# Optimization experiments

Measured on AMD Instinct MI355X. Metric: run time of the kernel, lower is better.

## Reference

```python
import jax, jax.numpy as jnp
import numpy as np

N = 10000        # num_nodes
F_IN = 256       # dataset_num_features
H = 128          # hidden_channels
C_OUT = 40       # dataset_num_classes
L = 3            # num_layers
HEADS = 8
DH = H // HEADS  # per-head dim
E = 160000       # num edges (before self loops)
SCALE = 1.0 / float(np.sqrt(DH))


def setup_inputs() -> dict:
    key = jax.random.key(0)
    ks = jax.random.split(key, 8)
    s = lambda k, *sh: (jax.random.normal(k, sh, dtype=jnp.float32) * 0.05)
    return dict(
        edge_index=jax.random.randint(ks[0], (2, E), 0, N, dtype=jnp.int32),
        x_param=s(ks[1], N, F_IN),
        lin1_w=s(ks[2], F_IN, H),
        lin1_b=jnp.zeros((H,), jnp.float32),
        wq=s(ks[3], L, H, H),
        wk=s(ks[4], L, H, H),
        wv=s(ks[5], L, H, H),
        bq=jnp.zeros((L, H), jnp.float32),
        bk=jnp.zeros((L, H), jnp.float32),
        bv=jnp.zeros((L, H), jnp.float32),
        lin2_w=s(ks[6], H, C_OUT),
        lin2_b=jnp.zeros((C_OUT,), jnp.float32),
    )


def _gcn_norm(edge_index):
    # PyG gcn_norm: add self loops (weight 1), symmetric D^-1/2 A D^-1/2
    loops = jnp.arange(N, dtype=edge_index.dtype)
    row = jnp.concatenate([edge_index[0], loops])  # source j
    col = jnp.concatenate([edge_index[1], loops])  # target i
    deg = jax.ops.segment_sum(jnp.ones(row.shape, jnp.float32), col, num_segments=N)
    dis = jnp.where(deg > 0, jax.lax.rsqrt(jnp.maximum(deg, 1e-12)), 0.0)
    return row, col, dis[row] * dis[col]


def _restricted_softmax(score):
    # softmax with an implicit extra logit at `margin=0`
    m = jnp.maximum(jnp.max(score, axis=-1, keepdims=True), 0.0)
    e = jnp.exp(score - m)
    return e / (jnp.sum(e, axis=-1, keepdims=True) + jnp.exp(-m))


def _forward(edge_index, x_param, lin1_w, lin1_b, wq, wk, wv, bq, bk, bv, lin2_w, lin2_b):
    row, col, norm = _gcn_norm(edge_index)
    # dropouts are eval-mode no-ops
    x = jax.nn.relu(x_param @ lin1_w + lin1_b)  # [N, H]
    x_all = x[:, None, :]                       # [N, 1, H]
    for l in range(L):
        t = x_all.shape[1]
        # project per-node first (linear commutes with per-edge gather)
        q = (x_all[:, -1] @ wq[l] + bq[l]).reshape(N, HEADS, DH)      # query from latest state
        k = (x_all @ wk[l] + bk[l]).reshape(N, t, HEADS, DH)          # keys over full history
        v = (x_all @ wv[l] + bv[l]).reshape(N, t, HEADS, DH)
        qe = q[col]   # [Etot, heads, dh]   (x_i)
        ke = k[row]   # [Etot, t, heads, dh] (x_j)
        ve = v[row]
        score = jnp.einsum('ehd,ethd->eht', qe, ke) * SCALE
        attn = _restricted_softmax(score)        # attention-dropout is a no-op in eval
        msg = jnp.einsum('eht,ethd->ehd', attn, ve).reshape(-1, H) * norm[:, None]
        out = jax.ops.segment_sum(msg, col, num_segments=N)  # aggr='add'
        x = jax.nn.relu(out)
        x_all = jnp.concatenate([x_all, x[:, None, :]], axis=1)
    logits = x_all[:, -1] @ lin2_w + lin2_b
    return jax.nn.log_softmax(logits, axis=1)


def reference(edge_index, x_param, lin1_w, lin1_b, wq, wk, wv, bq, bk, bv, lin2_w, lin2_b):
    return _forward(edge_index, x_param, lin1_w, lin1_b, wq, wk, wv, bq, bk, bv, lin2_w, lin2_b)
```

## Files before the change

kernel.cpp:

```cpp
#include <hip/hip_runtime.h>
#include <math.h>

#define N_NODES 10000
#define F_IN_D  256
#define H_DIM   128
#define C_OUTD  40
#define NHEADS  8
#define NEDGES  160000
#define ETOT    (NEDGES + N_NODES)
#define SCALE_F 0.25f
#define TILES_N 157
#define KVSZ    ((size_t)N_NODES * 3 * 256)

typedef __attribute__((ext_vector_type(8))) short bf16x8;
typedef __attribute__((ext_vector_type(4))) float f32x4;
typedef __attribute__((ext_vector_type(2))) float f32x2;

__device__ __forceinline__ unsigned short f2bf(float f) {
    unsigned int u = __float_as_uint(f);
    unsigned int r = (u + 0x7FFFu + ((u >> 16) & 1u)) >> 16;
    return (unsigned short)r;
}
__device__ __forceinline__ unsigned char f2fp8(float v) {
    int pk = __builtin_amdgcn_cvt_pk_fp8_f32(v, v, 0, false);
    return (unsigned char)(pk & 0xff);
}


__global__ void k_prep(const float* __restrict__ w1, const float* __restrict__ wq,
                       const float* __restrict__ wk, const float* __restrict__ wv,
                       const float* __restrict__ w2, const int* __restrict__ col,
                       unsigned short* __restrict__ W1T, unsigned short* __restrict__ WTq,
                       unsigned short* __restrict__ WTk, unsigned short* __restrict__ WTv,
                       unsigned short* __restrict__ W2T, int* __restrict__ degi) {
    int b = blockIdx.x;
    if (b < 728) {
        int e = b * 256 + threadIdx.x;
        if (e < 32768) {
            int n = e >> 8, k = e & 255;
            W1T[e] = f2bf(w1[k * H_DIM + n]);
        } else if (e < 180224) {
            int e2 = e - 32768;
            int mat = e2 >> 14;
            int r   = e2 & 16383;
            int n = r >> 7, k = r & 127;
            int l = mat / 3, ws = mat % 3;
            const float*    src = (ws == 0) ? wq  : (ws == 1) ? wk  : wv;
            unsigned short* dst = (ws == 0) ? WTq : (ws == 1) ? WTk : WTv;
            dst[l * 16384 + n * H_DIM + k] = f2bf(src[l * 16384 + k * H_DIM + n]);
        } else if (e < 186368) {
            int e3 = e - 180224;
            int c = e3 >> 7, k = e3 & 127;
            W2T[c * H_DIM + k] = (c < C_OUTD) ? f2bf(w2[k * C_OUTD + c]) : 0;
        }
    } else {
        int e = (b - 728) * 256 + threadIdx.x;
        if (e < NEDGES) atomicAdd(&degi[col[e]], 1);
    }
}


__device__ __forceinline__ void lin1_block(int bid, int ct0, const float* __restrict__ X,
                                           const unsigned short* __restrict__ W1T,
                                           const float* __restrict__ b1,
                                           unsigned short* __restrict__ X0, int nct) {
    int tid = threadIdx.x;
    int wid = tid >> 6, lane = tid & 63;
    int m = lane & 15, quad = lane >> 4;
    int rowA = bid * 64 + wid * 16 + m;
    int rowc = rowA < N_NODES ? rowA : N_NODES - 1;
    bf16x8 af[8];
    const float* ap = X + (size_t)rowc * F_IN_D + quad * 8;
    #pragma unroll
    for (int s = 0; s < 8; ++s) {
        float4 lo = *(const float4*)(ap + s * 32);
        float4 hi = *(const float4*)(ap + s * 32 + 4);
        union { unsigned short u[8]; bf16x8 v; } pk;
        pk.u[0] = f2bf(lo.x); pk.u[1] = f2bf(lo.y);
        pk.u[2] = f2bf(lo.z); pk.u[3] = f2bf(lo.w);
        pk.u[4] = f2bf(hi.x); pk.u[5] = f2bf(hi.y);
        pk.u[6] = f2bf(hi.z); pk.u[7] = f2bf(hi.w);
        af[s] = pk.v;
    }
    int row0 = bid * 64 + wid * 16 + quad * 4;
    for (int ct = ct0; ct < ct0 + nct; ++ct) {
        int col = ct * 16 + m;
        const unsigned short* bp = W1T + (size_t)col * F_IN_D + quad * 8;
        f32x4 acc = {0.f, 0.f, 0.f, 0.f};
        #pragma unroll
        for (int s = 0; s < 8; ++s) {
            bf16x8 bfr = __builtin_bit_cast(bf16x8, *(const uint4*)(bp + s * 32));
            acc = __builtin_amdgcn_mfma_f32_16x16x32_bf16(af[s], bfr, acc, 0, 0, 0);
        }
        float bb = b1[col];
        #pragma unroll
        for (int rg = 0; rg < 4; ++rg) {
            int r = row0 + rg;
            if (r < N_NODES)
                X0[(size_t)r * H_DIM + col] = f2bf(fmaxf(acc[rg] + bb, 0.f));
        }
    }
}

__device__ __forceinline__ void qkv_block(int mi, int rt,
                                          const unsigned short* __restrict__ XHb,
                                          const unsigned short* __restrict__ WTq_l,
                                          const unsigned short* __restrict__ WTk_l,
                                          const unsigned short* __restrict__ WTv_l,
                                          const float* __restrict__ bq_l,
                                          const float* __restrict__ bk_l,
                                          const float* __restrict__ bv_l,
                                          unsigned short* __restrict__ Qb,
                                          unsigned char* __restrict__ KVb,
                                          int hasQ, int qslice, int nK, int sbase, int nct) {
    int tid = threadIdx.x;
    int wid = tid >> 6, lane = tid & 63;
    int m = lane & 15, quad = lane >> 4;
    const unsigned short* WT; const float* bias; int slice, mode;
    if (hasQ && mi == 0) { WT = WTq_l; bias = bq_l; slice = qslice; mode = 0; }
    else {
        int j = mi - hasQ;
        if (j < nK) { WT = WTk_l; bias = bk_l; slice = sbase + j;      mode = 1; }
        else        { WT = WTv_l; bias = bv_l; slice = sbase + j - nK; mode = 2; }
    }
    const unsigned short* A = XHb + (size_t)slice * N_NODES * H_DIM;
    int rowA = rt * 64 + wid * 16 + m;
    bf16x8 af[4];
    const unsigned short* ap = A + (size_t)rowA * H_DIM + quad * 8;
    #pragma unroll
    for (int s = 0; s < 4; ++s)
        af[s] = __builtin_bit_cast(bf16x8, *(const uint4*)(ap + s * 32));
    int row0 = rt * 64 + wid * 16 + quad * 4;
    int vofs = (mode == 2) ? 8 : 0;
    for (int cp = 0; cp < nct; ++cp) {
        int colA = cp * 32 + m;
        int colB = colA + 16;
        const unsigned short* bpA = WT + (size_t)colA * H_DIM + quad * 8;
        const unsigned short* bpB = WT + (size_t)colB * H_DIM + quad * 8;
        bf16x8 bA[4], bB[4];
        #pragma unroll
        for (int s = 0; s < 4; ++s) {
            bA[s] = __builtin_bit_cast(bf16x8, *(const uint4*)(bpA + s * 32));
            bB[s] = __builtin_bit_cast(bf16x8, *(const uint4*)(bpB + s * 32));
        }
        f32x4 accA = {0.f, 0.f, 0.f, 0.f};
        f32x4 accB = {0.f, 0.f, 0.f, 0.f};
        #pragma unroll
        for (int s = 0; s < 4; ++s) {
            accA = __builtin_amdgcn_mfma_f32_16x16x32_bf16(af[s], bA[s], accA, 0, 0, 0);
            accB = __builtin_amdgcn_mfma_f32_16x16x32_bf16(af[s], bB[s], accB, 0, 0, 0);
        }
        float bbA = bias[colA], bbB = bias[colB];
        #pragma unroll
        for (int rg = 0; rg < 4; ++rg) {
            int r = row0 + rg;
            if (r < N_NODES) {
                float vA = accA[rg] + bbA;
                float vB = accB[rg] + bbB;
                if (mode == 0) {
                    Qb[(size_t)r * H_DIM + colA] = f2bf(vA * SCALE_F);
                    Qb[(size_t)r * H_DIM + colB] = f2bf(vB * SCALE_F);
                } else {
                    size_t nb = ((size_t)r * 3 + slice) * 256;
                    KVb[nb + (colA >> 3) * 16 + (colA & 7) + vofs] = f2fp8(vA);
                    KVb[nb + (colB >> 3) * 16 + (colB & 7) + vofs] = f2fp8(vB);
                }
            }
        }
    }
}


template <int T>
__device__ __forceinline__ void kv_load(const uint4* __restrict__ KV, int r, int ci,
                                        uint4 (&kv)[T]) {
    const uint4* p = KV + (size_t)r * 48 + ci;
    #pragma unroll
    for (int s = 0; s < T; ++s) kv[s] = p[s * 16];
}

template <int T>
__device__ __forceinline__ void edge_accum(const uint4 (&kv)[T], const float (&q)[8],
                                           float nrm, float (&a)[8]) {
    float den = 1.f;
    float mv[8];
    #pragma unroll
    for (int i = 0; i < 8; ++i) mv[i] = 0.f;
    #pragma unroll
    for (int s = 0; s < T; ++s) {
        f32x2 k0 = __builtin_amdgcn_cvt_pk_f32_fp8(kv[s].x, false);
        f32x2 k1 = __builtin_amdgcn_cvt_pk_f32_fp8(kv[s].x, true);
        f32x2 k2 = __builtin_amdgcn_cvt_pk_f32_fp8(kv[s].y, false);
        f32x2 k3 = __builtin_amdgcn_cvt_pk_f32_fp8(kv[s].y, true);
        float p = q[0] * k0[0] + q[1] * k0[1] + q[2] * k1[0] + q[3] * k1[1]
                + q[4] * k2[0] + q[5] * k2[1] + q[6] * k3[0] + q[7] * k3[1];
        p += __shfl_xor(p, 1, 2);
        float w = __expf(p);
        den += w;
        f32x2 v0 = __builtin_amdgcn_cvt_pk_f32_fp8(kv[s].z, false);
        f32x2 v1 = __builtin_amdgcn_cvt_pk_f32_fp8(kv[s].z, true);
        f32x2 v2 = __builtin_amdgcn_cvt_pk_f32_fp8(kv[s].w, false);
        f32x2 v3 = __builtin_amdgcn_cvt_pk_f32_fp8(kv[s].w, true);
        mv[0] += w * v0[0]; mv[1] += w * v0[1];
        mv[2] += w * v1[0]; mv[3] += w * v1[1];
        mv[4] += w * v2[0]; mv[5] += w * v2[1];
        mv[6] += w * v3[0]; mv[7] += w * v3[1];
    }
    float ws = __fdividef(nrm, den);
    #pragma unroll
    for (int i = 0; i < 8; ++i) a[i] += ws * mv[i];
}

template <int T>
__device__ __forceinline__ void attn_block(int bid, const unsigned short* __restrict__ Q,
                                           const uint4* __restrict__ KV,
                                           const int2* __restrict__ csr,
                                           const int* __restrict__ degi,
                                           unsigned int* __restrict__ Xout) {
    int tid = threadIdx.x;
    int wid = tid >> 6, lane = tid & 63;
    int quarter = lane >> 4, ci = lane & 15;
    int n = bid * 4 + wid;

    int cnt = degi[n] + 1;
    if (cnt > 64) cnt = 64;
    int li = lane < cnt ? lane : cnt - 1;
    int2 eAll = csr[(n << 6) + li];
    int   rAll = eAll.x;
    float nAll = (lane < cnt) ? __int_as_float(eAll.y) : 0.f;

    float q[8];
    {
        uint4 qp = *(const uint4*)&Q[(size_t)n * H_DIM + ci * 8];
        q[0] = __uint_as_float(qp.x << 16);
        q[1] = __uint_as_float(qp.x & 0xffff0000u);
        q[2] = __uint_as_float(qp.y << 16);
        q[3] = __uint_as_float(qp.y & 0xffff0000u);
        q[4] = __uint_as_float(qp.z << 16);
        q[5] = __uint_as_float(qp.z & 0xffff0000u);
        q[6] = __uint_as_float(qp.w << 16);
        q[7] = __uint_as_float(qp.w & 0xffff0000u);
    }
    int nq = (cnt + 3) >> 2;
    float a[8];
    #pragma unroll
    for (int i = 0; i < 8; ++i) a[i] = 0.f;

    auto rowN = [&](int j4) { return __shfl(rAll, j4 < 63 ? j4 : 63, 64); };
    auto nrmN = [&](int j4) { return __shfl(nAll, j4 < 63 ? j4 : 63, 64); };

    uint4 kv0[T], kv1[T], kv2[T];
    kv_load<T>(KV, rowN(quarter), ci, kv0);
    kv_load<T>(KV, rowN(4 + quarter), ci, kv1);
    kv_load<T>(KV, rowN(8 + quarter), ci, kv2);

    int j = 0;
    for (;;) {
        edge_accum<T>(kv0, q, nrmN(j * 4 + quarter), a);
        if (++j >= nq) break;
        kv_load<T>(KV, rowN((j + 2) * 4 + quarter), ci, kv0);
        edge_accum<T>(kv1, q, nrmN(j * 4 + quarter), a);
        if (++j >= nq) break;
        kv_load<T>(KV, rowN((j + 2) * 4 + quarter), ci, kv1);
        edge_accum<T>(kv2, q, nrmN(j * 4 + quarter), a);
        if (++j >= nq) break;
        kv_load<T>(KV, rowN((j + 2) * 4 + quarter), ci, kv2);
    }

    #pragma unroll
    for (int i = 0; i < 8; ++i) {
        a[i] += __shfl_xor(a[i], 16, 64);
        a[i] += __shfl_xor(a[i], 32, 64);
    }
    if (quarter == 0) {
        uint4 o;
        o.x = ((unsigned int)f2bf(fmaxf(a[1], 0.f)) << 16) | (unsigned int)f2bf(fmaxf(a[0], 0.f));
        o.y = ((unsigned int)f2bf(fmaxf(a[3], 0.f)) << 16) | (unsigned int)f2bf(fmaxf(a[2], 0.f));
        o.z = ((unsigned int)f2bf(fmaxf(a[5], 0.f)) << 16) | (unsigned int)f2bf(fmaxf(a[4], 0.f));
        o.w = ((unsigned int)f2bf(fmaxf(a[7], 0.f)) << 16) | (unsigned int)f2bf(fmaxf(a[6], 0.f));
        *(uint4*)&Xout[(size_t)n * 64 + ci * 4] = o;
    }
}


__global__ __launch_bounds__(256) void k_lin1_scatter(const float* __restrict__ X,
                                                      const unsigned short* __restrict__ W1T,
                                                      const float* __restrict__ b1,
                                                      unsigned short* __restrict__ X0,
                                                      const int* __restrict__ row,
                                                      const int* __restrict__ col,
                                                      const int* __restrict__ degi,
                                                      int* __restrict__ cursor,
                                                      int2* __restrict__ csr, int nct) {
    int b = blockIdx.x;
    if (b < 2 * TILES_N) {
        int rt = b % TILES_N, half = b / TILES_N;
        lin1_block(rt, half * 4, X, W1T, b1, X0, nct);
        return;
    }
    int e = (b - 2 * TILES_N) * 256 + threadIdx.x;
    if (e >= ETOT) return;
    int r, c;
    if (e < NEDGES) { r = row[e]; c = col[e]; }
    else            { r = c = e - NEDGES; }
    int slot = atomicAdd(&cursor[c], 1);
    if (slot > 63) slot = 63;
    float dr = rsqrtf((float)(degi[r] + 1));
    float dc = rsqrtf((float)(degi[c] + 1));
    int2 ent; ent.x = r; ent.y = __float_as_int(dr * dc);
    csr[(c << 6) + slot] = ent;
}

template <int T>
__global__ __launch_bounds__(256) void k_attn_qkvold(const unsigned short* __restrict__ Q,
                                                     const uint4* __restrict__ KV,
                                                     const int2* __restrict__ csr,
                                                     const int* __restrict__ degi,
                                                     unsigned int* __restrict__ Xout,
                                                     const unsigned short* __restrict__ XHb,
                                                     const unsigned short* __restrict__ WTk_l,
                                                     const unsigned short* __restrict__ WTv_l,
                                                     const float* __restrict__ bk_l,
                                                     const float* __restrict__ bv_l,
                                                     unsigned char* __restrict__ KVnext,
                                                     int nK, int nct) {
    if (blockIdx.x < 2500) {
        attn_block<T>(blockIdx.x, Q, KV, csr, degi, Xout);
        return;
    }
    int b = blockIdx.x - 2500;
    qkv_block(b / TILES_N, b % TILES_N, XHb, nullptr, WTk_l, WTv_l,
              nullptr, bk_l, bv_l, nullptr, KVnext, 0, 0, nK, 0, nct);
}

__global__ __launch_bounds__(256) void k_qkv(const unsigned short* __restrict__ XHb,
                                             const unsigned short* __restrict__ WTq_l,
                                             const unsigned short* __restrict__ WTk_l,
                                             const unsigned short* __restrict__ WTv_l,
                                             const float* __restrict__ bq_l,
                                             const float* __restrict__ bk_l,
                                             const float* __restrict__ bv_l,
                                             unsigned short* __restrict__ Qb,
                                             unsigned char* __restrict__ KVb,
                                             int qslice, int nct) {
    qkv_block(blockIdx.x / TILES_N, blockIdx.x % TILES_N, XHb, WTq_l, WTk_l, WTv_l,
              bq_l, bk_l, bv_l, Qb, KVb, 1, qslice, 1, qslice, nct);
}

template <int T>
__global__ __launch_bounds__(256) void k_attn_agg(const unsigned short* __restrict__ Q,
                                                  const uint4* __restrict__ KV,
                                                  const int2* __restrict__ csr,
                                                  const int* __restrict__ degi,
                                                  unsigned int* __restrict__ Xout) {
    attn_block<T>(blockIdx.x, Q, KV, csr, degi, Xout);
}


__global__ __launch_bounds__(128) void k_lin2_mfma(const unsigned short* __restrict__ X,
                                                   const unsigned short* __restrict__ W2T,
                                                   const float* __restrict__ b2,
                                                   float* __restrict__ out) {
    int tid = threadIdx.x;
    int wid = tid >> 6, lane = tid & 63;
    int m = lane & 15, quad = lane >> 4;
    int rowA = blockIdx.x * 32 + wid * 16 + m;
    bf16x8 af[4];
    const unsigned short* ap = X + (size_t)rowA * H_DIM + quad * 8;
    #pragma unroll
    for (int s = 0; s < 4; ++s)
        af[s] = __builtin_bit_cast(bf16x8, *(const uint4*)(ap + s * 32));

    f32x4 acc0 = {0.f, 0.f, 0.f, 0.f};
    f32x4 acc1 = {0.f, 0.f, 0.f, 0.f};
    f32x4 acc2 = {0.f, 0.f, 0.f, 0.f};
    const unsigned short* bp0 = W2T + (size_t)(m)      * H_DIM + quad * 8;
    const unsigned short* bp1 = W2T + (size_t)(16 + m) * H_DIM + quad * 8;
    const unsigned short* bp2 = W2T + (size_t)(32 + m) * H_DIM + quad * 8;
    #pragma unroll
    for (int s = 0; s < 4; ++s) {
        bf16x8 b0 = __builtin_bit_cast(bf16x8, *(const uint4*)(bp0 + s * 32));
        acc0 = __builtin_amdgcn_mfma_f32_16x16x32_bf16(af[s], b0, acc0, 0, 0, 0);
        bf16x8 b1 = __builtin_bit_cast(bf16x8, *(const uint4*)(bp1 + s * 32));
        acc1 = __builtin_amdgcn_mfma_f32_16x16x32_bf16(af[s], b1, acc1, 0, 0, 0);
        bf16x8 b2f = __builtin_bit_cast(bf16x8, *(const uint4*)(bp2 + s * 32));
        acc2 = __builtin_amdgcn_mfma_f32_16x16x32_bf16(af[s], b2f, acc2, 0, 0, 0);
    }

    float bb0 = b2[m], bb1 = b2[16 + m];
    float bb2 = (m < 8) ? b2[32 + m] : 0.f;
    int row0 = blockIdx.x * 32 + wid * 16 + quad * 4;
    #pragma unroll
    for (int rg = 0; rg < 4; ++rg) {
        int r = row0 + rg;
        float v0 = acc0[rg] + bb0;
        float v1 = acc1[rg] + bb1;
        float v2 = (m < 8) ? (acc2[rg] + bb2) : -INFINITY;
        float mx = fmaxf(fmaxf(v0, v1), v2);
        #pragma unroll
        for (int o = 8; o > 0; o >>= 1) mx = fmaxf(mx, __shfl_xor(mx, o, 16));
        float sm = __expf(v0 - mx) + __expf(v1 - mx) + ((m < 8) ? __expf(v2 - mx) : 0.f);
        #pragma unroll
        for (int o = 8; o > 0; o >>= 1) sm += __shfl_xor(sm, o, 16);
        float lse = mx + __logf(sm);
        if (r < N_NODES) {
            out[(size_t)r * C_OUTD + m]      = v0 - lse;
            out[(size_t)r * C_OUTD + 16 + m] = v1 - lse;
            if (m < 8) out[(size_t)r * C_OUTD + 32 + m] = v2 - lse;
        }
    }
}


extern "C" void kernel_launch(void* const* d_in, const int* in_sizes, int n_in,
                              void* d_out, int out_size, void* d_ws, size_t ws_size,
                              hipStream_t stream) {
    const int*   ei      = (const int*)d_in[0];
    const int*   row     = ei;
    const int*   col     = ei + NEDGES;
    const float* x_param = (const float*)d_in[1];
    const float* lin1_w  = (const float*)d_in[2];
    const float* lin1_b  = (const float*)d_in[3];
    const float* wq      = (const float*)d_in[4];
    const float* wk      = (const float*)d_in[5];
    const float* wv      = (const float*)d_in[6];
    const float* bq      = (const float*)d_in[7];
    const float* bk      = (const float*)d_in[8];
    const float* bv      = (const float*)d_in[9];
    const float* lin2_w  = (const float*)d_in[10];
    const float* lin2_b  = (const float*)d_in[11];
    float*       out     = (float*)d_out;

    char* wbase = (char*)d_ws;
    size_t off = 0;
    auto alloc = [&](size_t bytes) -> void* {
        off = (off + 255) & ~(size_t)255;
        void* p = wbase + off;
        off += bytes;
        return p;
    };
    int*            degi     = (int*)           alloc((size_t)N_NODES * 4);
    int*            cursor   = (int*)           alloc((size_t)N_NODES * 4);
    int2*           csr      = (int2*)          alloc((size_t)N_NODES * 64 * 8);
    unsigned short* W1T      = (unsigned short*)alloc((size_t)H_DIM * F_IN_D * 2);
    unsigned short* WTq      = (unsigned short*)alloc((size_t)3 * H_DIM * H_DIM * 2);
    unsigned short* WTk      = (unsigned short*)alloc((size_t)3 * H_DIM * H_DIM * 2);
    unsigned short* WTv      = (unsigned short*)alloc((size_t)3 * H_DIM * H_DIM * 2);
    unsigned short* W2T      = (unsigned short*)alloc((size_t)48 * H_DIM * 2);
    unsigned short* XHb      = (unsigned short*)alloc((size_t)4 * N_NODES * H_DIM * 2);
    unsigned short* Qb       = (unsigned short*)alloc((size_t)N_NODES * H_DIM * 2);
    unsigned char*  KVb      = (unsigned char*) alloc(2 * KVSZ);

    hipMemsetAsync(degi, 0,
                   (size_t)((char*)(cursor + N_NODES) - (char*)degi), stream);
    k_prep<<<1353, 256, 0, stream>>>(lin1_w, wq, wk, wv, lin2_w, col,
                                     W1T, WTq, WTk, WTv, W2T, degi);

    k_lin1_scatter<<<2 * TILES_N + 665, 256, 0, stream>>>(
        x_param, W1T, lin1_b, XHb, row, col, degi, cursor, csr, 4);

    k_qkv<<<3 * TILES_N, 256, 0, stream>>>(
        XHb, WTq, WTk, WTv, bq, bk, bv, Qb, KVb, 0, 4);

    unsigned int* X1 = (unsigned int*)(XHb + (size_t)1 * N_NODES * H_DIM);
    unsigned int* X2 = (unsigned int*)(XHb + (size_t)2 * N_NODES * H_DIM);
    unsigned int* X3 = (unsigned int*)(XHb + (size_t)3 * N_NODES * H_DIM);

    k_attn_qkvold<1><<<2500 + 2 * TILES_N, 256, 0, stream>>>(
        Qb, (const uint4*)KVb, csr, degi, X1,
        XHb, WTk + 16384, WTv + 16384, bk + H_DIM, bv + H_DIM,
        KVb + KVSZ, 1, 4);

    k_qkv<<<3 * TILES_N, 256, 0, stream>>>(
        XHb, WTq + 16384, WTk + 16384, WTv + 16384,
        bq + H_DIM, bk + H_DIM, bv + H_DIM, Qb, KVb + KVSZ, 1, 4);

    k_attn_qkvold<2><<<2500 + 4 * TILES_N, 256, 0, stream>>>(
        Qb, (const uint4*)(KVb + KVSZ), csr, degi, X2,
        XHb, WTk + 2 * 16384, WTv + 2 * 16384, bk + 2 * H_DIM, bv + 2 * H_DIM,
        KVb, 2, 4);

    k_qkv<<<3 * TILES_N, 256, 0, stream>>>(
        XHb, WTq + 2 * 16384, WTk + 2 * 16384, WTv + 2 * 16384,
        bq + 2 * H_DIM, bk + 2 * H_DIM, bv + 2 * H_DIM, Qb, KVb, 2, 4);

    k_attn_agg<3><<<2500, 256, 0, stream>>>(Qb, (const uint4*)KVb, csr, degi, X3);

    k_lin2_mfma<<<313, 128, 0, stream>>>(XHb + (size_t)3 * N_NODES * H_DIM,
                                         W2T, lin2_b, out);
}
```

Measured before the change: 228.0 us.

## Fuse all stages into one persistent cooperative kernel with grid syncs

Replaces the sequence of nine kernel launches plus a memset with a single cooperative persistent kernel that loops over work units per stage and separates stages with grid-wide barriers. This removes per-launch overhead and the idle gaps between dependent kernels. In exchange, every stage runs on an occupancy-limited grid with grid.sync costs, and the larger fused kernel may use more registers and run at lower occupancy. The old multi-kernel path is kept as a fallback if the cooperative launch fails, and lin2 now uses 256-thread blocks.

```diff
diff --git a/kernel.cpp b/kernel.cpp
--- a/kernel.cpp
+++ b/kernel.cpp
@@ -1,5 +1,8 @@
 #include <hip/hip_runtime.h>
+#include <hip/hip_cooperative_groups.h>
 #include <math.h>
+
+namespace cg = cooperative_groups;
 
 #define N_NODES 10000
 #define F_IN_D  256
@@ -27,38 +30,61 @@
 }
 
 
-__global__ void k_prep(const float* __restrict__ w1, const float* __restrict__ wq,
-                       const float* __restrict__ wk, const float* __restrict__ wv,
-                       const float* __restrict__ w2, const int* __restrict__ col,
-                       unsigned short* __restrict__ W1T, unsigned short* __restrict__ WTq,
-                       unsigned short* __restrict__ WTk, unsigned short* __restrict__ WTv,
-                       unsigned short* __restrict__ W2T, int* __restrict__ degi) {
-    int b = blockIdx.x;
+struct MegaArgs {
+    const int* row; const int* col;
+    const float* x_param;
+    const float* w1; const float* b1;
+    const float* wq; const float* wk; const float* wv;
+    const float* bq; const float* bk; const float* bv;
+    const float* w2; const float* b2;
+    float* out;
+    int* degi; int* cursor; int2* csr;
+    unsigned short* W1T; unsigned short* WTq; unsigned short* WTk;
+    unsigned short* WTv; unsigned short* W2T; unsigned short* XHb;
+    unsigned short* Qb; unsigned char* KVb;
+    int nct;
+};
+
+
+__device__ __forceinline__ void prep_unit(int b, const MegaArgs& A) {
     if (b < 728) {
         int e = b * 256 + threadIdx.x;
         if (e < 32768) {
             int n = e >> 8, k = e & 255;
-            W1T[e] = f2bf(w1[k * H_DIM + n]);
+            A.W1T[e] = f2bf(A.w1[k * H_DIM + n]);
         } else if (e < 180224) {
             int e2 = e - 32768;
             int mat = e2 >> 14;
             int r   = e2 & 16383;
             int n = r >> 7, k = r & 127;
             int l = mat / 3, ws = mat % 3;
-            const float*    src = (ws == 0) ? wq  : (ws == 1) ? wk  : wv;
-            unsigned short* dst = (ws == 0) ? WTq : (ws == 1) ? WTk : WTv;
+            const float*    src = (ws == 0) ? A.wq  : (ws == 1) ? A.wk  : A.wv;
+            unsigned short* dst = (ws == 0) ? A.WTq : (ws == 1) ? A.WTk : A.WTv;
             dst[l * 16384 + n * H_DIM + k] = f2bf(src[l * 16384 + k * H_DIM + n]);
         } else if (e < 186368) {
             int e3 = e - 180224;
             int c = e3 >> 7, k = e3 & 127;
-            W2T[c * H_DIM + k] = (c < C_OUTD) ? f2bf(w2[k * C_OUTD + c]) : 0;
+            A.W2T[c * H_DIM + k] = (c < C_OUTD) ? f2bf(A.w2[k * C_OUTD + c]) : 0;
         }
     } else {
         int e = (b - 728) * 256 + threadIdx.x;
-        if (e < NEDGES) atomicAdd(&degi[col[e]], 1);
-    }
-}
-
+        if (e < NEDGES) atomicAdd(&A.degi[A.col[e]], 1);
+    }
+}
+
+__device__ __forceinline__ void scatter_unit(int su, const MegaArgs& A) {
+    int e = su * 256 + threadIdx.x;
+    if (e >= ETOT) return;
+    int r, c;
+    if (e < NEDGES) { r = A.row[e]; c = A.col[e]; }
+    else            { r = c = e - NEDGES; }
+    int slot = atomicAdd(&A.cursor[c], 1);
+    if (slot > 63) slot = 63;
+    float dr = rsqrtf((float)(A.degi[r] + 1));
+    float dc = rsqrtf((float)(A.degi[c] + 1));
+    int2 ent; ent.x = r; ent.y = __float_as_int(dr * dc);
+    A.csr[(c << 6) + slot] = ent;
+}
 
 __device__ __forceinline__ void lin1_block(int bid, int ct0, const float* __restrict__ X,
                                            const unsigned short* __restrict__ W1T,
@@ -282,89 +308,14 @@
     }
 }
 
-
-__global__ __launch_bounds__(256) void k_lin1_scatter(const float* __restrict__ X,
-                                                      const unsigned short* __restrict__ W1T,
-                                                      const float* __restrict__ b1,
-                                                      unsigned short* __restrict__ X0,
-                                                      const int* __restrict__ row,
-                                                      const int* __restrict__ col,
-                                                      const int* __restrict__ degi,
-                                                      int* __restrict__ cursor,
-                                                      int2* __restrict__ csr, int nct) {
-    int b = blockIdx.x;
-    if (b < 2 * TILES_N) {
-        int rt = b % TILES_N, half = b / TILES_N;
-        lin1_block(rt, half * 4, X, W1T, b1, X0, nct);
-        return;
-    }
-    int e = (b - 2 * TILES_N) * 256 + threadIdx.x;
-    if (e >= ETOT) return;
-    int r, c;
-    if (e < NEDGES) { r = row[e]; c = col[e]; }
-    else            { r = c = e - NEDGES; }
-    int slot = atomicAdd(&cursor[c], 1);
-    if (slot > 63) slot = 63;
-    float dr = rsqrtf((float)(degi[r] + 1));
-    float dc = rsqrtf((float)(degi[c] + 1));
-    int2 ent; ent.x = r; ent.y = __float_as_int(dr * dc);
-    csr[(c << 6) + slot] = ent;
-}
-
-template <int T>
-__global__ __launch_bounds__(256) void k_attn_qkvold(const unsigned short* __restrict__ Q,
-                                                     const uint4* __restrict__ KV,
-                                                     const int2* __restrict__ csr,
-                                                     const int* __restrict__ degi,
-                                                     unsigned int* __restrict__ Xout,
-                                                     const unsigned short* __restrict__ XHb,
-                                                     const unsigned short* __restrict__ WTk_l,
-                                                     const unsigned short* __restrict__ WTv_l,
-                                                     const float* __restrict__ bk_l,
-                                                     const float* __restrict__ bv_l,
-                                                     unsigned char* __restrict__ KVnext,
-                                                     int nK, int nct) {
-    if (blockIdx.x < 2500) {
-        attn_block<T>(blockIdx.x, Q, KV, csr, degi, Xout);
-        return;
-    }
-    int b = blockIdx.x - 2500;
-    qkv_block(b / TILES_N, b % TILES_N, XHb, nullptr, WTk_l, WTv_l,
-              nullptr, bk_l, bv_l, nullptr, KVnext, 0, 0, nK, 0, nct);
-}
-
-__global__ __launch_bounds__(256) void k_qkv(const unsigned short* __restrict__ XHb,
-                                             const unsigned short* __restrict__ WTq_l,
-                                             const unsigned short* __restrict__ WTk_l,
-                                             const unsigned short* __restrict__ WTv_l,
-                                             const float* __restrict__ bq_l,
-                                             const float* __restrict__ bk_l,
-                                             const float* __restrict__ bv_l,
-                                             unsigned short* __restrict__ Qb,
-                                             unsigned char* __restrict__ KVb,
-                                             int qslice, int nct) {
-    qkv_block(blockIdx.x / TILES_N, blockIdx.x % TILES_N, XHb, WTq_l, WTk_l, WTv_l,
-              bq_l, bk_l, bv_l, Qb, KVb, 1, qslice, 1, qslice, nct);
-}
-
-template <int T>
-__global__ __launch_bounds__(256) void k_attn_agg(const unsigned short* __restrict__ Q,
-                                                  const uint4* __restrict__ KV,
-                                                  const int2* __restrict__ csr,
-                                                  const int* __restrict__ degi,
-                                                  unsigned int* __restrict__ Xout) {
-    attn_block<T>(blockIdx.x, Q, KV, csr, degi, Xout);
-}
-
-
-__global__ __launch_bounds__(128) void k_lin2_mfma(const unsigned short* __restrict__ X,
-                                                   const unsigned short* __restrict__ W2T,
-                                                   const float* __restrict__ b2,
-                                                   float* __restrict__ out) {
+__device__ __forceinline__ void lin2_block(int bid, const unsigned short* __restrict__ X,
+                                           const unsigned short* __restrict__ W2T,
+                                           const float* __restrict__ b2,
+                                           float* __restrict__ out) {
     int tid = threadIdx.x;
     int wid = tid >> 6, lane = tid & 63;
     int m = lane & 15, quad = lane >> 4;
-    int rowA = blockIdx.x * 32 + wid * 16 + m;
+    int rowA = bid * 64 + wid * 16 + m;
     bf16x8 af[4];
     const unsigned short* ap = X + (size_t)rowA * H_DIM + quad * 8;
     #pragma unroll
@@ -389,7 +340,7 @@
 
     float bb0 = b2[m], bb1 = b2[16 + m];
     float bb2 = (m < 8) ? b2[32 + m] : 0.f;
-    int row0 = blockIdx.x * 32 + wid * 16 + quad * 4;
+    int row0 = bid * 64 + wid * 16 + quad * 4;
     #pragma unroll
     for (int rg = 0; rg < 4; ++rg) {
         int r = row0 + rg;
@@ -412,25 +363,129 @@
 }
 
 
+__global__ __launch_bounds__(256) void k_mega(MegaArgs A) {
+    cg::grid_group grid = cg::this_grid();
+    const int nb  = gridDim.x;
+    const int gt  = blockIdx.x * 256 + threadIdx.x;
+    const int gsz = nb * 256;
+
+    unsigned int* X1 = (unsigned int*)(A.XHb + (size_t)1 * N_NODES * H_DIM);
+    unsigned int* X2 = (unsigned int*)(A.XHb + (size_t)2 * N_NODES * H_DIM);
+    unsigned int* X3 = (unsigned int*)(A.XHb + (size_t)3 * N_NODES * H_DIM);
+
+    for (int i = gt; i < N_NODES; i += gsz) { A.degi[i] = 0; A.cursor[i] = 0; }
+    grid.sync();
+
+    for (int u = blockIdx.x; u < 1353; u += nb) prep_unit(u, A);
+    grid.sync();
+
+    for (int u = blockIdx.x; u < 979; u += nb) {
+        if (u < 314) lin1_block(u % TILES_N, (u / TILES_N) * 4,
+                                A.x_param, A.W1T, A.b1, A.XHb, A.nct);
+        else scatter_unit(u - 314, A);
+    }
+    grid.sync();
+
+    for (int u = blockIdx.x; u < 471; u += nb)
+        qkv_block(u / TILES_N, u % TILES_N, A.XHb, A.WTq, A.WTk, A.WTv,
+                  A.bq, A.bk, A.bv, A.Qb, A.KVb, 1, 0, 1, 0, A.nct);
+    grid.sync();
+
+    for (int u = blockIdx.x; u < 2814; u += nb) {
+        if (u < 2500) attn_block<1>(u, A.Qb, (const uint4*)A.KVb, A.csr, A.degi, X1);
+        else {
+            int b = u - 2500;
+            qkv_block(b / TILES_N, b % TILES_N, A.XHb, nullptr,
+                      A.WTk + 16384, A.WTv + 16384, nullptr,
+                      A.bk + H_DIM, A.bv + H_DIM, nullptr,
+                      A.KVb + KVSZ, 0, 0, 1, 0, A.nct);
+        }
+    }
+    grid.sync();
+
+    for (int u = blockIdx.x; u < 471; u += nb)
+        qkv_block(u / TILES_N, u % TILES_N, A.XHb,
+                  A.WTq + 16384, A.WTk + 16384, A.WTv + 16384,
+                  A.bq + H_DIM, A.bk + H_DIM, A.bv + H_DIM,
+                  A.Qb, A.KVb + KVSZ, 1, 1, 1, 1, A.nct);
+    grid.sync();
+
+    for (int u = blockIdx.x; u < 3128; u += nb) {
+        if (u < 2500) attn_block<2>(u, A.Qb, (const uint4*)(A.KVb + KVSZ),
+                                    A.csr, A.degi, X2);
+        else {
+            int b = u - 2500;
+            qkv_block(b / TILES_N, b % TILES_N, A.XHb, nullptr,
+                      A.WTk + 32768, A.WTv + 32768, nullptr,
+                      A.bk + 2 * H_DIM, A.bv + 2 * H_DIM, nullptr,
+                      A.KVb, 0, 0, 2, 0, A.nct);
+        }
+    }
+    grid.sync();
+
+    for (int u = blockIdx.x; u < 471; u += nb)
+        qkv_block(u / TILES_N, u % TILES_N, A.XHb,
+                  A.WTq + 32768, A.WTk + 32768, A.WTv + 32768,
+                  A.bq + 2 * H_DIM, A.bk + 2 * H_DIM, A.bv + 2 * H_DIM,
+                  A.Qb, A.KVb, 1, 2, 1, 2, A.nct);
+    grid.sync();
+
+    for (int u = blockIdx.x; u < 2500; u += nb)
+        attn_block<3>(u, A.Qb, (const uint4*)A.KVb, A.csr, A.degi, X3);
+    grid.sync();
+
+    for (int u = blockIdx.x; u < TILES_N; u += nb)
+        lin2_block(u, A.XHb + (size_t)3 * N_NODES * H_DIM, A.W2T, A.b2, A.out);
+}
+
+
+__global__ void k_prep_f(MegaArgs A) { prep_unit(blockIdx.x, A); }
+
+__global__ __launch_bounds__(256) void k_lin1_scatter_f(MegaArgs A) {
+    int b = blockIdx.x;
+    if (b < 2 * TILES_N) lin1_block(b % TILES_N, (b / TILES_N) * 4,
+                                    A.x_param, A.W1T, A.b1, A.XHb, A.nct);
+    else scatter_unit(b - 2 * TILES_N, A);
+}
+
+__global__ __launch_bounds__(256) void k_qkv_f(MegaArgs A, int woff, int qslice) {
+    qkv_block(blockIdx.x / TILES_N, blockIdx.x % TILES_N, A.XHb,
+              A.WTq + woff, A.WTk + woff, A.WTv + woff,
+              A.bq + qslice * H_DIM, A.bk + qslice * H_DIM, A.bv + qslice * H_DIM,
+              A.Qb, A.KVb + (size_t)(qslice & 1) * KVSZ, 1, qslice, 1, qslice, A.nct);
+}
+
+template <int T>
+__global__ __launch_bounds__(256) void k_attn_qkvold_f(MegaArgs A, int l) {
+    unsigned int* Xo = (unsigned int*)(A.XHb + (size_t)(l + 1) * N_NODES * H_DIM);
+    const unsigned char* kvcur = A.KVb + (size_t)(l & 1) * KVSZ;
+    if (blockIdx.x < 2500) {
+        attn_block<T>(blockIdx.x, A.Qb, (const uint4*)kvcur, A.csr, A.degi, Xo);
+        return;
+    }
+    int b = blockIdx.x - 2500;
+    int woff = (l + 1) * 16384;
+    qkv_block(b / TILES_N, b % TILES_N, A.XHb, nullptr,
+              A.WTk + woff, A.WTv + woff, nullptr,
+              A.bk + (l + 1) * H_DIM, A.bv + (l + 1) * H_DIM, nullptr,
+              A.KVb + (size_t)((l + 1) & 1) * KVSZ, 0, 0, l + 1, 0, A.nct);
+}
+
+template <int T>
+__global__ __launch_bounds__(256) void k_attn_f(MegaArgs A, int l) {
+    unsigned int* Xo = (unsigned int*)(A.XHb + (size_t)(l + 1) * N_NODES * H_DIM);
+    const unsigned char* kvcur = A.KVb + (size_t)(l & 1) * KVSZ;
+    attn_block<T>(blockIdx.x, A.Qb, (const uint4*)kvcur, A.csr, A.degi, Xo);
+}
+
+__global__ __launch_bounds__(256) void k_lin2_f(MegaArgs A) {
+    lin2_block(blockIdx.x, A.XHb + (size_t)3 * N_NODES * H_DIM, A.W2T, A.b2, A.out);
+}
+
+
 extern "C" void kernel_launch(void* const* d_in, const int* in_sizes, int n_in,
                               void* d_out, int out_size, void* d_ws, size_t ws_size,
                               hipStream_t stream) {
-    const int*   ei      = (const int*)d_in[0];
-    const int*   row     = ei;
-    const int*   col     = ei + NEDGES;
-    const float* x_param = (const float*)d_in[1];
-    const float* lin1_w  = (const float*)d_in[2];
-    const float* lin1_b  = (const float*)d_in[3];
-    const float* wq      = (const float*)d_in[4];
-    const float* wk      = (const float*)d_in[5];
-    const float* wv      = (const float*)d_in[6];
-    const float* bq      = (const float*)d_in[7];
-    const float* bk      = (const float*)d_in[8];
-    const float* bv      = (const float*)d_in[9];
-    const float* lin2_w  = (const float*)d_in[10];
-    const float* lin2_b  = (const float*)d_in[11];
-    float*       out     = (float*)d_out;
-
     char* wbase = (char*)d_ws;
     size_t off = 0;
     auto alloc = [&](size_t bytes) -> void* {
@@ -439,53 +494,57 @@
         off += bytes;
         return p;
     };
-    int*            degi     = (int*)           alloc((size_t)N_NODES * 4);
-    int*            cursor   = (int*)           alloc((size_t)N_NODES * 4);
-    int2*           csr      = (int2*)          alloc((size_t)N_NODES * 64 * 8);
-    unsigned short* W1T      = (unsigned short*)alloc((size_t)H_DIM * F_IN_D * 2);
-    unsigned short* WTq      = (unsigned short*)alloc((size_t)3 * H_DIM * H_DIM * 2);
-    unsigned short* WTk      = (unsigned short*)alloc((size_t)3 * H_DIM * H_DIM * 2);
-    unsigned short* WTv      = (unsigned short*)alloc((size_t)3 * H_DIM * H_DIM * 2);
-    unsigned short* W2T      = (unsigned short*)alloc((size_t)48 * H_DIM * 2);
-    unsigned short* XHb      = (unsigned short*)alloc((size_t)4 * N_NODES * H_DIM * 2);
-    unsigned short* Qb       = (unsigned short*)alloc((size_t)N_NODES * H_DIM * 2);
-    unsigned char*  KVb      = (unsigned char*) alloc(2 * KVSZ);
-
-    hipMemsetAsync(degi, 0,
-                   (size_t)((char*)(cursor + N_NODES) - (char*)degi), stream);
-    k_prep<<<1353, 256, 0, stream>>>(lin1_w, wq, wk, wv, lin2_w, col,
-                                     W1T, WTq, WTk, WTv, W2T, degi);
-
-    k_lin1_scatter<<<2 * TILES_N + 665, 256, 0, stream>>>(
-        x_param, W1T, lin1_b, XHb, row, col, degi, cursor, csr, 4);
-
-    k_qkv<<<3 * TILES_N, 256, 0, stream>>>(
-        XHb, WTq, WTk, WTv, bq, bk, bv, Qb, KVb, 0, 4);
-
-    unsigned int* X1 = (unsigned int*)(XHb + (size_t)1 * N_NODES * H_DIM);
-    unsigned int* X2 = (unsigned int*)(XHb + (size_t)2 * N_NODES * H_DIM);
-    unsigned int* X3 = (unsigned int*)(XHb + (size_t)3 * N_NODES * H_DIM);
-
-    k_attn_qkvold<1><<<2500 + 2 * TILES_N, 256, 0, stream>>>(
-        Qb, (const uint4*)KVb, csr, degi, X1,
-        XHb, WTk + 16384, WTv + 16384, bk + H_DIM, bv + H_DIM,
-        KVb + KVSZ, 1, 4);
-
-    k_qkv<<<3 * TILES_N, 256, 0, stream>>>(
-        XHb, WTq + 16384, WTk + 16384, WTv + 16384,
-        bq + H_DIM, bk + H_DIM, bv + H_DIM, Qb, KVb + KVSZ, 1, 4);
-
-    k_attn_qkvold<2><<<2500 + 4 * TILES_N, 256, 0, stream>>>(
-        Qb, (const uint4*)(KVb + KVSZ), csr, degi, X2,
-        XHb, WTk + 2 * 16384, WTv + 2 * 16384, bk + 2 * H_DIM, bv + 2 * H_DIM,
-        KVb, 2, 4);
-
-    k_qkv<<<3 * TILES_N, 256, 0, stream>>>(
-        XHb, WTq + 2 * 16384, WTk + 2 * 16384, WTv + 2 * 16384,
-        bq + 2 * H_DIM, bk + 2 * H_DIM, bv + 2 * H_DIM, Qb, KVb, 2, 4);
-
-    k_attn_agg<3><<<2500, 256, 0, stream>>>(Qb, (const uint4*)KVb, csr, degi, X3);
-
-    k_lin2_mfma<<<313, 128, 0, stream>>>(XHb + (size_t)3 * N_NODES * H_DIM,
-                                         W2T, lin2_b, out);
-}
+    MegaArgs A;
+    A.row     = (const int*)d_in[0];
+    A.col     = (const int*)d_in[0] + NEDGES;
+    A.x_param = (const float*)d_in[1];
+    A.w1      = (const float*)d_in[2];
+    A.b1      = (const float*)d_in[3];
+    A.wq      = (const float*)d_in[4];
+    A.wk      = (const float*)d_in[5];
+    A.wv      = (const float*)d_in[6];
+    A.bq      = (const float*)d_in[7];
+    A.bk      = (const float*)d_in[8];
+    A.bv      = (const float*)d_in[9];
+    A.w2      = (const float*)d_in[10];
+    A.b2      = (const float*)d_in[11];
+    A.out     = (float*)d_out;
+    A.degi    = (int*)           alloc((size_t)N_NODES * 4);
+    A.cursor  = (int*)           alloc((size_t)N_NODES * 4);
+    A.csr     = (int2*)          alloc((size_t)N_NODES * 64 * 8);
+    A.W1T     = (unsigned short*)alloc((size_t)H_DIM * F_IN_D * 2);
+    A.WTq     = (unsigned short*)alloc((size_t)3 * H_DIM * H_DIM * 2);
+    A.WTk     = (unsigned short*)alloc((size_t)3 * H_DIM * H_DIM * 2);
+    A.WTv     = (unsigned short*)alloc((size_t)3 * H_DIM * H_DIM * 2);
+    A.W2T     = (unsigned short*)alloc((size_t)48 * H_DIM * 2);
+    A.XHb     = (unsigned short*)alloc((size_t)4 * N_NODES * H_DIM * 2);
+    A.Qb      = (unsigned short*)alloc((size_t)N_NODES * H_DIM * 2);
+    A.KVb     = (unsigned char*) alloc(2 * KVSZ);
+    A.nct     = 4;
+
+    static int nblk = 0;
+    if (nblk == 0) {
+        int per = 0;
+        hipOccupancyMaxActiveBlocksPerMultiprocessor(&per, k_mega, 256, 0);
+        if (per < 1) per = 1;
+        nblk = per * 256;
+        if (nblk > 2048) nblk = 2048;
+    }
+
+    void* kargs[] = { (void*)&A };
+    hipError_t err = hipLaunchCooperativeKernel((const void*)k_mega, dim3(nblk),
+                                                dim3(256), kargs, 0, stream);
+    if (err == hipSuccess) return;
+
+    hipMemsetAsync(A.degi, 0, (size_t)N_NODES * 4, stream);
+    hipMemsetAsync(A.cursor, 0, (size_t)N_NODES * 4, stream);
+    k_prep_f<<<1353, 256, 0, stream>>>(A);
+    k_lin1_scatter_f<<<2 * TILES_N + 665, 256, 0, stream>>>(A);
+    k_qkv_f<<<3 * TILES_N, 256, 0, stream>>>(A, 0, 0);
+    k_attn_qkvold_f<1><<<2500 + 2 * TILES_N, 256, 0, stream>>>(A, 0);
+    k_qkv_f<<<3 * TILES_N, 256, 0, stream>>>(A, 16384, 1);
+    k_attn_qkvold_f<2><<<2500 + 4 * TILES_N, 256, 0, stream>>>(A, 1);
+    k_qkv_f<<<3 * TILES_N, 256, 0, stream>>>(A, 32768, 2);
+    k_attn_f<3><<<2500, 256, 0, stream>>>(A, 2);
+    k_lin2_f<<<TILES_N, 256, 0, stream>>>(A);
+}
```

After: 777.9 us. 241% more time.
